# Optimization experiments

Hardware: AMD Instinct MI355X
Metric: run time of the kernel (lower is better)

The kernel has to match this reference:

```python
import jax, jax.numpy as jnp
import numpy as np

N_NODES = 100000
N_EDGES = 1250000
D_FEAT = 64


def setup_inputs() -> dict:
    key = jax.random.key(0)
    kx, ke = jax.random.split(key)
    x = jax.random.normal(kx, (N_NODES, D_FEAT), dtype=jnp.float32)
    edge_index = jax.random.randint(ke, (2, N_EDGES), 0, N_NODES, dtype=jnp.int64)
    return {"x": x, "edge_index": edge_index}


def _aggregate(x, src, dst, num_nodes):
    # out[i] = sum_{e: dst[e]==i} x[src[e]]  (identity message, 'add' aggr)
    return jax.ops.segment_sum(x[src], dst, num_segments=num_nodes)


def reference(x, edge_index):
    num_nodes = x.shape[0]
    src, dst = edge_index[0], edge_index[1]  # PyG source_to_target flow
    h = _aggregate(x, src, dst, num_nodes)   # conv1
    h = jax.nn.relu(h)
    h = _aggregate(h, src, dst, num_nodes)   # conv2
    return h
```

## Files before the change

### kernel.cpp

```cpp
#include <hip/hip_runtime.h>
#include <hip/hip_bf16.h>


#define N_FEAT    64
#define BIN_SHIFT 7
#define BIN_NODES 128
#define CAPBIN    2048
#define NB_H      784
#define NSCAN     1024
#define GSTRIDE   16
#define TILE      4096
#define NPTR      (BIN_NODES + 1)
#define SRCSH     14

typedef unsigned int u32;
typedef unsigned short u16;
typedef __attribute__((ext_vector_type(8))) unsigned short u16x8;
typedef __attribute__((ext_vector_type(4))) unsigned int u32x4;
typedef __attribute__((ext_vector_type(2))) float f32x2;

__device__ inline u16 f2bf(float f) {
    u32 u = __builtin_bit_cast(u32, f);
    return (u16)((u + 0x7FFFu + ((u >> 16) & 1u)) >> 16);
}

__global__ __launch_bounds__(256) void partition_convert_kernel(
    const float* __restrict__ xf, u16* __restrict__ xb, int n_elems,
    const int* __restrict__ src, const int* __restrict__ dst,
    u32* __restrict__ gcur,
    u32* __restrict__ cbdata,
    int n_edges, int n_bins, int part_blocks)
{
    __shared__ u32 hist[NSCAN];
    __shared__ u32 starts[NSCAN];
    __shared__ u32 lpos[NSCAN];
    __shared__ u32 wcur[NB_H];
    __shared__ u32 sortbuf[TILE];
    __shared__ u16 binid[TILE];
    __shared__ u32 wsum[4];

    const int tid = threadIdx.x;

    if ((int)blockIdx.x >= part_blocks) {
        int i = (((int)blockIdx.x - part_blocks) * 256 + tid) * 8;
        if (i < n_elems) {
            float4 a = *(const float4*)(xf + i);
            float4 b = *(const float4*)(xf + i + 4);
            u16x8 r;
            r[0]=f2bf(a.x); r[1]=f2bf(a.y); r[2]=f2bf(a.z); r[3]=f2bf(a.w);
            r[4]=f2bf(b.x); r[5]=f2bf(b.y); r[6]=f2bf(b.z); r[7]=f2bf(b.w);
            *(u16x8*)(xb + i) = r;
        }
        return;
    }

    const int tbase = (int)blockIdx.x * TILE;
    const int tend  = min(tbase + TILE, n_edges);

    for (int i = tid; i < NSCAN; i += 256) { hist[i] = 0; lpos[i] = 0; }
    __syncthreads();

    for (int e = tbase + tid; e < tend; e += 256)
        atomicAdd(&hist[(u32)dst[e] >> BIN_SHIFT], 1u);
    __syncthreads();

    {
        const int b0 = tid * 4;
        u32 h0 = hist[b0], h1 = hist[b0+1], h2 = hist[b0+2], h3 = hist[b0+3];
        u32 s  = h0 + h1 + h2 + h3;
        u32 inc = s;
        #pragma unroll
        for (int d = 1; d < 64; d <<= 1) {
            u32 o = __shfl_up(inc, d);
            if ((tid & 63) >= d) inc += o;
        }
        if ((tid & 63) == 63) wsum[tid >> 6] = inc;
        __syncthreads();
        u32 woff = 0;
        #pragma unroll
        for (int k = 0; k < 4; ++k) if (k < (tid >> 6)) woff += wsum[k];
        u32 excl = woff + inc - s;
        starts[b0]   = excl;
        starts[b0+1] = excl + h0;
        starts[b0+2] = excl + h0 + h1;
        starts[b0+3] = excl + h0 + h1 + h2;
    }
    __syncthreads();

    const int rot = (int)(((u32)blockIdx.x * 193u) % (u32)n_bins);
    for (int i = tid; i < n_bins; i += 256) {
        int b = i + rot; if (b >= n_bins) b -= n_bins;
        u32 h = hist[b];
        if (h) wcur[b] = atomicAdd(&gcur[b * GSTRIDE], h);
    }
    __syncthreads();

    for (int e = tbase + tid; e < tend; e += 256) {
        int d = dst[e];
        int s = src[e];
        u32 b   = (u32)d >> BIN_SHIFT;
        u32 pos = starts[b] + atomicAdd(&lpos[b], 1u);
        sortbuf[pos] = ((u32)(d & (BIN_NODES - 1)) << 17) | (u32)s;
        binid[pos]   = (u16)b;
    }
    __syncthreads();

    const int cnt = tend - tbase;
    for (int j = tid; j < cnt; j += 256) {
        u32 b   = binid[j];
        u32 rel = wcur[b] + ((u32)j - starts[b]);
        if (rel < CAPBIN)
            cbdata[(size_t)b * CAPBIN + rel] = sortbuf[j];
    }
}

__global__ __launch_bounds__(256) void bin_sort_kernel(
    u32* __restrict__ cbdata,
    const u32* __restrict__ gcur,
    u32* __restrict__ nodeptr,
    int n_bins)
{
    __shared__ u32 hist[NSCAN];
    __shared__ u32 starts[NSCAN];
    __shared__ u32 lpos[NSCAN];
    __shared__ u32 sl[CAPBIN];
    __shared__ u32 wsum[4];

    const int tid = threadIdx.x;
    const int bin = blockIdx.x;
    if (bin >= n_bins) return;

    for (int i = tid; i < NSCAN; i += 256) { hist[i] = 0; lpos[i] = 0; }
    __syncthreads();

    int cnt = (int)gcur[bin * GSTRIDE];
    if (cnt > CAPBIN) cnt = CAPBIN;
    u32* bd = cbdata + (size_t)bin * CAPBIN;

    for (int j = tid; j < cnt; j += 256) {
        u32 p = bd[j];
        u32 key = ((p >> 17) << 3) | ((p & 0x1FFFFu) >> SRCSH);
        atomicAdd(&hist[key], 1u);
    }
    __syncthreads();

    {
        const int b0 = tid * 4;
        u32 h0 = hist[b0], h1 = hist[b0+1], h2 = hist[b0+2], h3 = hist[b0+3];
        u32 s  = h0 + h1 + h2 + h3;
        u32 inc = s;
        #pragma unroll
        for (int d = 1; d < 64; d <<= 1) {
            u32 o = __shfl_up(inc, d);
            if ((tid & 63) >= d) inc += o;
        }
        if ((tid & 63) == 63) wsum[tid >> 6] = inc;
        __syncthreads();
        u32 woff = 0;
        #pragma unroll
        for (int k = 0; k < 4; ++k) if (k < (tid >> 6)) woff += wsum[k];
        u32 excl = woff + inc - s;
        starts[b0]   = excl;
        starts[b0+1] = excl + h0;
        starts[b0+2] = excl + h0 + h1;
        starts[b0+3] = excl + h0 + h1 + h2;
    }
    __syncthreads();

    for (int j = tid; j < cnt; j += 256) {
        u32 p   = bd[j];
        u32 key = ((p >> 17) << 3) | ((p & 0x1FFFFu) >> SRCSH);
        u32 pos = starts[key] + atomicAdd(&lpos[key], 1u);
        sl[pos] = p & 0x1FFFFu;
    }
    __syncthreads();

    const u32 base = (u32)bin * CAPBIN;
    for (int j = tid; j < cnt; j += 256)
        bd[j] = sl[j];
    if (tid < BIN_NODES)
        nodeptr[(size_t)bin * NPTR + tid] = base + starts[tid << 3];
    if (tid == 0)
        nodeptr[(size_t)bin * NPTR + BIN_NODES] = base + (u32)cnt;
}

__global__ __launch_bounds__(256) void aggregate_kernel(
    const u16* __restrict__ xin,
    const u32* __restrict__ csorted,
    const u32* __restrict__ nodeptr,
    u16* __restrict__ out_bf,
    float* __restrict__ out_f,
    int n_nodes, int pass)
{
    const int tid  = threadIdx.x;

    const int w    = tid >> 6;
    const int lane = tid & 63;
    const int grp  = lane >> 3;
    const int sub  = lane & 7;
    const char* xc = (const char*)xin;

    const int nl   = w * 8 + grp;
    const int node = (int)blockIdx.x * 32 + nl;
    const int bin  = node >> BIN_SHIFT;
    const int nid  = node & (BIN_NODES - 1);

    const int s0  = (int)nodeptr[(size_t)bin * NPTR + nid];
    const int s1  = (int)nodeptr[(size_t)bin * NPTR + nid + 1];

    f32x2 a0={0.f,0.f}, a1={0.f,0.f}, a2={0.f,0.f}, a3={0.f,0.f};

    int jb = s0;
    for (; jb + 8 <= s1; jb += 8) {
        u32 myid = csorted[jb + sub];
        #pragma unroll
        for (int k = 0; k < 8; ++k) {
            u32 s = (u32)__shfl((int)myid, (lane & 56) + k, 64);
            u32x4 v = *(const u32x4*)(xc + ((size_t)s << 7) + (sub << 4));
            a0 += (f32x2){ __builtin_bit_cast(float, v[0] << 16),
                           __builtin_bit_cast(float, v[0] & 0xFFFF0000u) };
            a1 += (f32x2){ __builtin_bit_cast(float, v[1] << 16),
                           __builtin_bit_cast(float, v[1] & 0xFFFF0000u) };
            a2 += (f32x2){ __builtin_bit_cast(float, v[2] << 16),
                           __builtin_bit_cast(float, v[2] & 0xFFFF0000u) };
            a3 += (f32x2){ __builtin_bit_cast(float, v[3] << 16),
                           __builtin_bit_cast(float, v[3] & 0xFFFF0000u) };
        }
    }
    if (jb < s1) {
        u32 myid = 0;
        if (jb + sub < s1) myid = csorted[jb + sub];
        const int m = s1 - jb;
        #pragma unroll 1
        for (int k = 0; k < m; ++k) {
            u32 s = (u32)__shfl((int)myid, (lane & 56) + k, 64);
            u32x4 v = *(const u32x4*)(xc + ((size_t)s << 7) + (sub << 4));
            a0 += (f32x2){ __builtin_bit_cast(float, v[0] << 16),
                           __builtin_bit_cast(float, v[0] & 0xFFFF0000u) };
            a1 += (f32x2){ __builtin_bit_cast(float, v[1] << 16),
                           __builtin_bit_cast(float, v[1] & 0xFFFF0000u) };
            a2 += (f32x2){ __builtin_bit_cast(float, v[2] << 16),
                           __builtin_bit_cast(float, v[2] & 0xFFFF0000u) };
            a3 += (f32x2){ __builtin_bit_cast(float, v[3] << 16),
                           __builtin_bit_cast(float, v[3] & 0xFFFF0000u) };
        }
    }

    if (node < n_nodes) {
        if (pass == 0) {
            u16x8 o;
            o[0]=f2bf(fmaxf(a0.x,0.f)); o[1]=f2bf(fmaxf(a0.y,0.f));
            o[2]=f2bf(fmaxf(a1.x,0.f)); o[3]=f2bf(fmaxf(a1.y,0.f));
            o[4]=f2bf(fmaxf(a2.x,0.f)); o[5]=f2bf(fmaxf(a2.y,0.f));
            o[6]=f2bf(fmaxf(a3.x,0.f)); o[7]=f2bf(fmaxf(a3.y,0.f));
            *(u16x8*)(out_bf + (size_t)node * N_FEAT + sub * 8) = o;
        } else {
            float* dp = out_f + (size_t)node * N_FEAT + sub * 8;
            *(float4*)dp       = (float4){a0.x, a0.y, a1.x, a1.y};
            *(float4*)(dp + 4) = (float4){a2.x, a2.y, a3.x, a3.y};
        }
    }
}

extern "C" void kernel_launch(void* const* d_in, const int* in_sizes, int n_in,
                              void* d_out, int out_size, void* d_ws, size_t ws_size,
                              hipStream_t stream) {
    const float* x          = (const float*)d_in[0];
    const int*   edge_index = (const int*)d_in[1];

    const int n_edges = in_sizes[1] / 2;
    const int* src = edge_index;
    const int* dst = edge_index + n_edges;

    const int n_nodes = out_size / N_FEAT;
    const int n_bins  = (n_nodes + BIN_NODES - 1) >> BIN_SHIFT;
    float* out = (float*)d_out;

    const size_t xb_bytes    = (size_t)out_size * sizeof(u16);
    const size_t hb_bytes    = (size_t)out_size * sizeof(u16);
    const size_t cb_bytes    = (size_t)n_bins * CAPBIN * sizeof(u32);
    const size_t np_bytes    = (size_t)n_bins * NPTR * sizeof(u32);
    const size_t gcur_bytes  = (size_t)NB_H * GSTRIDE * sizeof(u32);

    char* w = (char*)d_ws;
    u16* xb      = (u16*)w;              w += xb_bytes;
    u16* hb      = (u16*)w;              w += hb_bytes;
    u32* cbdata  = (u32*)w;              w += cb_bytes;
    u32* nodeptr = (u32*)w;              w += np_bytes;
    u32* gcur    = (u32*)w;

    hipMemsetAsync(gcur, 0, gcur_bytes, stream);

    const int part_blocks = (n_edges + TILE - 1) / TILE;
    const int conv_blocks = (out_size / 8 + 255) / 256;
    partition_convert_kernel<<<part_blocks + conv_blocks, 256, 0, stream>>>(
        x, xb, out_size, src, dst, gcur, cbdata, n_edges, n_bins, part_blocks);

    bin_sort_kernel<<<n_bins, 256, 0, stream>>>(cbdata, gcur, nodeptr, n_bins);

    const int agg_blocks = (n_nodes + 31) / 32;
    aggregate_kernel<<<agg_blocks, 256, 0, stream>>>(xb, cbdata, nodeptr, hb, nullptr, n_nodes, 0);
    aggregate_kernel<<<agg_blocks, 256, 0, stream>>>(hb, cbdata, nodeptr, nullptr, out, n_nodes, 1);
}
```

Measured before the change: 162.6 us.

## Split convert from partition and hold edge data in registers across passes

```diff
diff --git a/kernel.cpp b/kernel.cpp
--- a/kernel.cpp
+++ b/kernel.cpp
@@ -10,6 +10,7 @@
 #define NSCAN     1024
 #define GSTRIDE   16
 #define TILE      4096
+#define EPT       16
 #define NPTR      (BIN_NODES + 1)
 #define SRCSH     14
 
@@ -24,12 +25,25 @@
     return (u16)((u + 0x7FFFu + ((u >> 16) & 1u)) >> 16);
 }
 
-__global__ __launch_bounds__(256) void partition_convert_kernel(
-    const float* __restrict__ xf, u16* __restrict__ xb, int n_elems,
+__global__ __launch_bounds__(256) void convert_kernel(
+    const float* __restrict__ xf, u16* __restrict__ xb, int n_elems)
+{
+    int i = ((int)blockIdx.x * 256 + (int)threadIdx.x) * 8;
+    if (i < n_elems) {
+        float4 a = *(const float4*)(xf + i);
+        float4 b = *(const float4*)(xf + i + 4);
+        u16x8 r;
+        r[0]=f2bf(a.x); r[1]=f2bf(a.y); r[2]=f2bf(a.z); r[3]=f2bf(a.w);
+        r[4]=f2bf(b.x); r[5]=f2bf(b.y); r[6]=f2bf(b.z); r[7]=f2bf(b.w);
+        *(u16x8*)(xb + i) = r;
+    }
+}
+
+__global__ __launch_bounds__(256) void partition_kernel(
     const int* __restrict__ src, const int* __restrict__ dst,
     u32* __restrict__ gcur,
     u32* __restrict__ cbdata,
-    int n_edges, int n_bins, int part_blocks)
+    int n_edges, int n_bins)
 {
     __shared__ u32 hist[NSCAN];
     __shared__ u32 starts[NSCAN];
@@ -39,29 +53,27 @@
     __shared__ u16 binid[TILE];
     __shared__ u32 wsum[4];
 
-    const int tid = threadIdx.x;
-
-    if ((int)blockIdx.x >= part_blocks) {
-        int i = (((int)blockIdx.x - part_blocks) * 256 + tid) * 8;
-        if (i < n_elems) {
-            float4 a = *(const float4*)(xf + i);
-            float4 b = *(const float4*)(xf + i + 4);
-            u16x8 r;
-            r[0]=f2bf(a.x); r[1]=f2bf(a.y); r[2]=f2bf(a.z); r[3]=f2bf(a.w);
-            r[4]=f2bf(b.x); r[5]=f2bf(b.y); r[6]=f2bf(b.z); r[7]=f2bf(b.w);
-            *(u16x8*)(xb + i) = r;
-        }
-        return;
-    }
-
+    const int tid   = threadIdx.x;
     const int tbase = (int)blockIdx.x * TILE;
     const int tend  = min(tbase + TILE, n_edges);
 
     for (int i = tid; i < NSCAN; i += 256) { hist[i] = 0; lpos[i] = 0; }
     __syncthreads();
 
-    for (int e = tbase + tid; e < tend; e += 256)
-        atomicAdd(&hist[(u32)dst[e] >> BIN_SHIFT], 1u);
+    u32 breg[EPT];
+    u32 preg[EPT];
+    #pragma unroll
+    for (int k = 0; k < EPT; ++k) {
+        int e = tbase + tid + k * 256;
+        breg[k] = ~0u;
+        if (e < tend) {
+            int d = dst[e];
+            int s = src[e];
+            breg[k] = (u32)d >> BIN_SHIFT;
+            preg[k] = ((u32)(d & (BIN_NODES - 1)) << 17) | (u32)s;
+            atomicAdd(&hist[breg[k]], 1u);
+        }
+    }
     __syncthreads();
 
     {
@@ -95,13 +107,14 @@
     }
     __syncthreads();
 
-    for (int e = tbase + tid; e < tend; e += 256) {
-        int d = dst[e];
-        int s = src[e];
-        u32 b   = (u32)d >> BIN_SHIFT;
-        u32 pos = starts[b] + atomicAdd(&lpos[b], 1u);
-        sortbuf[pos] = ((u32)(d & (BIN_NODES - 1)) << 17) | (u32)s;
-        binid[pos]   = (u16)b;
+    #pragma unroll
+    for (int k = 0; k < EPT; ++k) {
+        if (breg[k] != ~0u) {
+            u32 b   = breg[k];
+            u32 pos = starts[b] + atomicAdd(&lpos[b], 1u);
+            sortbuf[pos] = preg[k];
+            binid[pos]   = (u16)b;
+        }
     }
     __syncthreads();
 
@@ -291,10 +304,12 @@
 
     hipMemsetAsync(gcur, 0, gcur_bytes, stream);
 
+    const int conv_blocks = (out_size / 8 + 255) / 256;
+    convert_kernel<<<conv_blocks, 256, 0, stream>>>(x, xb, out_size);
+
     const int part_blocks = (n_edges + TILE - 1) / TILE;
-    const int conv_blocks = (out_size / 8 + 255) / 256;
-    partition_convert_kernel<<<part_blocks + conv_blocks, 256, 0, stream>>>(
-        x, xb, out_size, src, dst, gcur, cbdata, n_edges, n_bins, part_blocks);
+    partition_kernel<<<part_blocks, 256, 0, stream>>>(
+        src, dst, gcur, cbdata, n_edges, n_bins);
 
     bin_sort_kernel<<<n_bins, 256, 0, stream>>>(cbdata, gcur, nodeptr, n_bins);
 
```

Result: no change. 163.6 us (+0.6%).
